# Kernel tuning notes

Hardware: AMD Instinct MI355X
Metric: run time of the kernel (lower is better)

The kernel has to match this reference:

```python
import jax, jax.numpy as jnp
import numpy as np

SPACING = 2
EPS = 1e-8

def setup_inputs() -> dict:
    key = jax.random.key(0)
    x = jax.random.normal(key, (32, 96, 128, 128), dtype=jnp.float32)
    return {"hidden_activations": x}

def reference(hidden_activations):
    s = SPACING
    B, C, H, W = hidden_activations.shape
    ph, pw = H // s, W // s
    R = ph * pw
    # F.unfold(kernel=s, stride=s) -> regions [B,C,R,s*s], kernel positions row-major
    regions = hidden_activations.reshape(B, C, ph, s, pw, s)
    regions = regions.transpose(0, 1, 2, 4, 3, 5).reshape(B, C, R, s * s)
    # append null (no-winner) logit = 0
    aug = jnp.concatenate([regions, jnp.zeros((B, C, R, 1), regions.dtype)], axis=-1)
    # stabilized softmax with +eps in denominator (as in torch code)
    m = jnp.max(aug, axis=-1, keepdims=True)
    e = jnp.exp(aug - m)
    probs = e / (jnp.sum(e, axis=-1, keepdims=True) + EPS)  # [B,C,R,s*s+1]
    # Gumbel-argmax sampling of one winner per region (or null)
    gkey = jax.random.key(1)
    u = jax.random.uniform(gkey, probs.shape, dtype=probs.dtype)
    gumbel = -jnp.log(-jnp.log(u + EPS) + EPS)
    winner = jnp.argmax(jnp.log(probs + EPS) + gumbel, axis=-1)  # [B,C,R]
    # probability value at winner location
    winner_prob = jnp.take_along_axis(probs, winner[..., None], axis=-1)  # [B,C,R,1]
    # scatter winner prob into full-resolution sparse map; winner==s*s (null) -> all zeros
    onehot = (winner[..., None] == jnp.arange(s * s)).astype(probs.dtype)  # [B,C,R,s*s]
    sparse = (onehot * winner_prob).reshape(B, C, ph, pw, s, s)
    sparse = sparse.transpose(0, 1, 2, 4, 3, 5).reshape(B, C, H, W)
    # MATLAB HPc: sum of non-null probs per region
    pooled = jnp.sum(probs[..., :-1], axis=-1).reshape(B, C, ph, pw)
    winner_indices = winner.reshape(B, C, ph, pw)
    return sparse, pooled, winner_indices
```

## Files before the change

kernel.cpp:

```cpp
#include <hip/hip_runtime.h>
#include <stdint.h>

static constexpr uint32_t kBC       = 32u * 96u;
static constexpr uint32_t kR        = 64u * 64u;
static constexpr uint32_t kImg      = 128u * 128u;
static constexpr uint32_t kSparseN  = kBC * kImg;
static constexpr uint32_t kPooledN  = kBC * kR;

#define EPSF 1e-8f

__device__ __forceinline__ uint32_t rotl32(uint32_t v, int r) {
    return (v << r) | (v >> (32 - r));
}

__device__ __forceinline__ void threefry2x32_01(uint32_t x0, uint32_t x1,
                                                uint32_t& o0, uint32_t& o1) {
    const uint32_t ks0 = 0u;
    const uint32_t ks1 = 1u;
    const uint32_t ks2 = 0x1BD11BDAu ^ 0u ^ 1u;
    x0 += ks0; x1 += ks1;
    x0 += x1; x1 = rotl32(x1, 13); x1 ^= x0;
    x0 += x1; x1 = rotl32(x1, 15); x1 ^= x0;
    x0 += x1; x1 = rotl32(x1, 26); x1 ^= x0;
    x0 += x1; x1 = rotl32(x1,  6); x1 ^= x0;
    x0 += ks1; x1 += ks2 + 1u;
    x0 += x1; x1 = rotl32(x1, 17); x1 ^= x0;
    x0 += x1; x1 = rotl32(x1, 29); x1 ^= x0;
    x0 += x1; x1 = rotl32(x1, 16); x1 ^= x0;
    x0 += x1; x1 = rotl32(x1, 24); x1 ^= x0;
    x0 += ks2; x1 += ks0 + 2u;
    x0 += x1; x1 = rotl32(x1, 13); x1 ^= x0;
    x0 += x1; x1 = rotl32(x1, 15); x1 ^= x0;
    x0 += x1; x1 = rotl32(x1, 26); x1 ^= x0;
    x0 += x1; x1 = rotl32(x1,  6); x1 ^= x0;
    x0 += ks0; x1 += ks1 + 3u;
    x0 += x1; x1 = rotl32(x1, 17); x1 ^= x0;
    x0 += x1; x1 = rotl32(x1, 29); x1 ^= x0;
    x0 += x1; x1 = rotl32(x1, 16); x1 ^= x0;
    x0 += x1; x1 = rotl32(x1, 24); x1 ^= x0;
    x0 += ks1; x1 += ks2 + 4u;
    x0 += x1; x1 = rotl32(x1, 13); x1 ^= x0;
    x0 += x1; x1 = rotl32(x1, 15); x1 ^= x0;
    x0 += x1; x1 = rotl32(x1, 26); x1 ^= x0;
    x0 += x1; x1 = rotl32(x1,  6); x1 ^= x0;
    x0 += ks2; x1 += ks0 + 5u;
    o0 = x0; o1 = x1;
}

__device__ __forceinline__ uint32_t jax_bits_partitionable(uint32_t i) {
    uint32_t o0, o1;
    threefry2x32_01(0u, i, o0, o1);
    return o0 ^ o1;
}

__device__ __forceinline__ float gumbel_from_bits(uint32_t bits) {
    uint32_t fb = (bits >> 9) | 0x3F800000u;
    float u = __uint_as_float(fb) - 1.0f;
    float nl = -logf(u + EPSF);
    return -logf(nl + EPSF);
}

__device__ __forceinline__ void do_region_fused(float v0, float v1, float v2, float v3,
                                                uint32_t jbase5,
                                                float& s0, float& s1, float& s2, float& s3,
                                                float& pooledv, float& winv) {
    float g0 = gumbel_from_bits(jax_bits_partitionable(jbase5 + 0u));
    float g1 = gumbel_from_bits(jax_bits_partitionable(jbase5 + 1u));
    float g2 = gumbel_from_bits(jax_bits_partitionable(jbase5 + 2u));
    float g3 = gumbel_from_bits(jax_bits_partitionable(jbase5 + 3u));
    float g4 = gumbel_from_bits(jax_bits_partitionable(jbase5 + 4u));

    float m = fmaxf(fmaxf(fmaxf(fmaxf(v0, v1), v2), v3), 0.0f);
    float e0 = expf(v0 - m);
    float e1 = expf(v1 - m);
    float e2 = expf(v2 - m);
    float e3 = expf(v3 - m);
    float e4 = expf(0.0f - m);
    float den = ((((e0 + e1) + e2) + e3) + e4) + EPSF;
    float p0 = e0 / den;
    float p1 = e1 / den;
    float p2 = e2 / den;
    float p3 = e3 / den;
    float p4 = e4 / den;
    float z0 = logf(p0 + EPSF) + g0;
    float z1 = logf(p1 + EPSF) + g1;
    float z2 = logf(p2 + EPSF) + g2;
    float z3 = logf(p3 + EPSF) + g3;
    float z4 = logf(p4 + EPSF) + g4;
    int w = 0; float best = z0;
    if (z1 > best) { best = z1; w = 1; }
    if (z2 > best) { best = z2; w = 2; }
    if (z3 > best) { best = z3; w = 3; }
    if (z4 > best) { best = z4; w = 4; }
    float wp = (w == 0) ? p0 : (w == 1) ? p1 : (w == 2) ? p2 : (w == 3) ? p3 : p4;
    s0 = (w == 0) ? wp : 0.0f;
    s1 = (w == 1) ? wp : 0.0f;
    s2 = (w == 2) ? wp : 0.0f;
    s3 = (w == 3) ? wp : 0.0f;
    pooledv = ((p0 + p1) + p2) + p3;
    winv = (float)w;
}

__global__ __launch_bounds__(256, 6) void mmp_kernel(const float* __restrict__ x,
                                                     float* __restrict__ sparse,
                                                     float* __restrict__ pooled,
                                                     float* __restrict__ winner) {
    const uint32_t t  = blockIdx.x * 256u + threadIdx.x;
    const uint32_t pj = t & 15u;
    const uint32_t pi = (t >> 4) & 63u;
    const uint32_t bc = t >> 10;

    const float* xp = x + (size_t)bc * kImg + pi * 256u + pj * 8u;
    float4 a0 = *(const float4*)(xp);
    float4 a1 = *(const float4*)(xp + 4);
    float4 b0 = *(const float4*)(xp + 128);
    float4 b1 = *(const float4*)(xp + 132);

    const uint32_t r0    = bc * kR + pi * 64u + pj * 4u;
    const uint32_t jbase = r0 * 5u;
    float* sp = sparse + (size_t)bc * kImg + pi * 256u + pj * 8u;

    float s0, s1, s2, s3;
    float pool0, pool1, pool2, pool3, win0, win1, win2, win3;

    do_region_fused(a0.x, a0.y, b0.x, b0.y, jbase,       s0, s1, s2, s3, pool0, win0);
    *(float2*)(sp)           = make_float2(s0, s1);
    *(float2*)(sp + 128)     = make_float2(s2, s3);
    do_region_fused(a0.z, a0.w, b0.z, b0.w, jbase + 5u,  s0, s1, s2, s3, pool1, win1);
    *(float2*)(sp + 2)       = make_float2(s0, s1);
    *(float2*)(sp + 130)     = make_float2(s2, s3);
    do_region_fused(a1.x, a1.y, b1.x, b1.y, jbase + 10u, s0, s1, s2, s3, pool2, win2);
    *(float2*)(sp + 4)       = make_float2(s0, s1);
    *(float2*)(sp + 132)     = make_float2(s2, s3);
    do_region_fused(a1.z, a1.w, b1.z, b1.w, jbase + 15u, s0, s1, s2, s3, pool3, win3);
    *(float2*)(sp + 6)       = make_float2(s0, s1);
    *(float2*)(sp + 134)     = make_float2(s2, s3);

    *(float4*)(pooled + r0) = make_float4(pool0, pool1, pool2, pool3);
    *(float4*)(winner + r0) = make_float4(win0, win1, win2, win3);
}

extern "C" void kernel_launch(void* const* d_in, const int* in_sizes, int n_in,
                              void* d_out, int out_size, void* d_ws, size_t ws_size,
                              hipStream_t stream) {
    (void)in_sizes; (void)n_in; (void)d_ws; (void)ws_size; (void)out_size;
    const float* x = (const float*)d_in[0];
    float* out = (float*)d_out;
    float* sparse = out;
    float* pooled = out + kSparseN;
    float* winner = out + kSparseN + kPooledN;

    const uint32_t nThreads = kBC * 64u * 16u;
    dim3 grid(nThreads / 256u), block(256u);
    hipLaunchKernelGGL(mmp_kernel, grid, block, 0, stream, x, sparse, pooled, winner);
}
```

Before: 491.7 us.

## Use hardware log2/exp2/rcp fast path with exact fixup pass for ambiguous regions

Replaces precise expf/logf/division in the main kernel with the AMD hardware exp2, log2 and reciprocal intrinsics, and computes the Gumbel-argmax in log2 space. Regions where the top-two margin is small, the input spread is large, or a uniform sample is near zero are pushed onto a workspace list through an atomic counter. A second kernel recomputes those regions with full-precision math to keep the reference winners. This adds a memset, an extra launch and atomic contention in exchange for cheaper transcendental math, and if the list overflows its capacity some regions are left on the approximate path.

```diff
diff --git a/kernel.cpp b/kernel.cpp
--- a/kernel.cpp
+++ b/kernel.cpp
@@ -8,6 +8,9 @@
 static constexpr uint32_t kPooledN  = kBC * kR;
 
 #define EPSF 1e-8f
+#define GAP_THR2 2e-3f
+#define SPREAD_THR 7.0f
+#define TMIN_THR 1e-5f
 
 __device__ __forceinline__ uint32_t rotl32(uint32_t v, int r) {
     return (v << r) | (v >> (32 - r));
@@ -53,45 +56,74 @@
     return o0 ^ o1;
 }
 
-__device__ __forceinline__ float gumbel_from_bits(uint32_t bits) {
+__device__ __forceinline__ float uniform_from_bits(uint32_t bits) {
     uint32_t fb = (bits >> 9) | 0x3F800000u;
-    float u = __uint_as_float(fb) - 1.0f;
-    float nl = -logf(u + EPSF);
-    return -logf(nl + EPSF);
-}
-
-__device__ __forceinline__ void do_region_fused(float v0, float v1, float v2, float v3,
-                                                uint32_t jbase5,
-                                                float& s0, float& s1, float& s2, float& s3,
-                                                float& pooledv, float& winv) {
-    float g0 = gumbel_from_bits(jax_bits_partitionable(jbase5 + 0u));
-    float g1 = gumbel_from_bits(jax_bits_partitionable(jbase5 + 1u));
-    float g2 = gumbel_from_bits(jax_bits_partitionable(jbase5 + 2u));
-    float g3 = gumbel_from_bits(jax_bits_partitionable(jbase5 + 3u));
-    float g4 = gumbel_from_bits(jax_bits_partitionable(jbase5 + 4u));
-
-    float m = fmaxf(fmaxf(fmaxf(fmaxf(v0, v1), v2), v3), 0.0f);
-    float e0 = expf(v0 - m);
-    float e1 = expf(v1 - m);
-    float e2 = expf(v2 - m);
-    float e3 = expf(v3 - m);
-    float e4 = expf(0.0f - m);
+    return __uint_as_float(fb) - 1.0f;
+}
+
+__device__ __forceinline__ float hw_log2(float x) { return __builtin_amdgcn_logf(x); }
+__device__ __forceinline__ float hw_exp2(float x) { return __builtin_amdgcn_exp2f(x); }
+__device__ __forceinline__ float hw_rcp (float x) { return __builtin_amdgcn_rcpf(x); }
+
+__device__ __forceinline__ void do_region_v5(float v0, float v1, float v2, float v3,
+                                             uint32_t rIdx,
+                                             uint32_t* wcount, uint32_t* wlist, uint32_t cap,
+                                             float& s0, float& s1, float& s2, float& s3,
+                                             float& pooledv, float& winv) {
+    const uint32_t jb = rIdx * 5u;
+    float u0 = uniform_from_bits(jax_bits_partitionable(jb + 0u));
+    float u1 = uniform_from_bits(jax_bits_partitionable(jb + 1u));
+    float u2 = uniform_from_bits(jax_bits_partitionable(jb + 2u));
+    float u3 = uniform_from_bits(jax_bits_partitionable(jb + 3u));
+    float u4 = uniform_from_bits(jax_bits_partitionable(jb + 4u));
+
+    const float L2E  = 1.44269504088896340736f;
+    const float NLN2 = -0.69314718055994530942f;
+
+    float m    = fmaxf(fmaxf(fmaxf(fmaxf(v0, v1), v2), v3), 0.0f);
+    float vmin = fminf(fminf(v0, v1), fminf(v2, v3));
+    float c0 = v0 * L2E, c1 = v1 * L2E, c2 = v2 * L2E, c3 = v3 * L2E;
+    float cm = m * L2E;
+
+    float e0 = hw_exp2(c0 - cm);
+    float e1 = hw_exp2(c1 - cm);
+    float e2 = hw_exp2(c2 - cm);
+    float e3 = hw_exp2(c3 - cm);
+    float e4 = hw_exp2(0.0f - cm);
     float den = ((((e0 + e1) + e2) + e3) + e4) + EPSF;
-    float p0 = e0 / den;
-    float p1 = e1 / den;
-    float p2 = e2 / den;
-    float p3 = e3 / den;
-    float p4 = e4 / den;
-    float z0 = logf(p0 + EPSF) + g0;
-    float z1 = logf(p1 + EPSF) + g1;
-    float z2 = logf(p2 + EPSF) + g2;
-    float z3 = logf(p3 + EPSF) + g3;
-    float z4 = logf(p4 + EPSF) + g4;
-    int w = 0; float best = z0;
-    if (z1 > best) { best = z1; w = 1; }
-    if (z2 > best) { best = z2; w = 2; }
-    if (z3 > best) { best = z3; w = 3; }
-    if (z4 > best) { best = z4; w = 4; }
+    float rr  = hw_rcp(den);
+    float p0 = e0 * rr;
+    float p1 = e1 * rr;
+    float p2 = e2 * rr;
+    float p3 = e3 * rr;
+    float p4 = e4 * rr;
+
+    float t0 = fmaf(NLN2, hw_log2(u0 + EPSF), EPSF);
+    float t1 = fmaf(NLN2, hw_log2(u1 + EPSF), EPSF);
+    float t2 = fmaf(NLN2, hw_log2(u2 + EPSF), EPSF);
+    float t3 = fmaf(NLN2, hw_log2(u3 + EPSF), EPSF);
+    float t4 = fmaf(NLN2, hw_log2(u4 + EPSF), EPSF);
+    float z0 = c0 - hw_log2(t0);
+    float z1 = c1 - hw_log2(t1);
+    float z2 = c2 - hw_log2(t2);
+    float z3 = c3 - hw_log2(t3);
+    float z4 = 0.0f - hw_log2(t4);
+    float tmin = fminf(fminf(fminf(t0, t1), fminf(t2, t3)), t4);
+
+    int w = 0; float best = z0; float second = -3.4e38f;
+    if (z1 > best) { second = best; best = z1; w = 1; } else { second = z1; }
+    if (z2 > best) { second = best; best = z2; w = 2; } else if (z2 > second) { second = z2; }
+    if (z3 > best) { second = best; best = z3; w = 3; } else if (z3 > second) { second = z3; }
+    if (z4 > best) { second = best; best = z4; w = 4; } else if (z4 > second) { second = z4; }
+
+    bool flag = (best - second < GAP_THR2) ||
+                (m - fminf(vmin, 0.0f) > SPREAD_THR) ||
+                (tmin < TMIN_THR);
+    if (flag) {
+        uint32_t slot = atomicAdd(wcount, 1u);
+        if (slot < cap) wlist[slot] = rIdx;
+    }
+
     float wp = (w == 0) ? p0 : (w == 1) ? p1 : (w == 2) ? p2 : (w == 3) ? p3 : p4;
     s0 = (w == 0) ? wp : 0.0f;
     s1 = (w == 1) ? wp : 0.0f;
@@ -104,7 +136,10 @@
 __global__ __launch_bounds__(256, 6) void mmp_kernel(const float* __restrict__ x,
                                                      float* __restrict__ sparse,
                                                      float* __restrict__ pooled,
-                                                     float* __restrict__ winner) {
+                                                     float* __restrict__ winner,
+                                                     uint32_t* __restrict__ wcount,
+                                                     uint32_t* __restrict__ wlist,
+                                                     uint32_t cap) {
     const uint32_t t  = blockIdx.x * 256u + threadIdx.x;
     const uint32_t pj = t & 15u;
     const uint32_t pi = (t >> 4) & 63u;
@@ -116,41 +151,104 @@
     float4 b0 = *(const float4*)(xp + 128);
     float4 b1 = *(const float4*)(xp + 132);
 
-    const uint32_t r0    = bc * kR + pi * 64u + pj * 4u;
-    const uint32_t jbase = r0 * 5u;
+    const uint32_t r0 = bc * kR + pi * 64u + pj * 4u;
     float* sp = sparse + (size_t)bc * kImg + pi * 256u + pj * 8u;
 
     float s0, s1, s2, s3;
     float pool0, pool1, pool2, pool3, win0, win1, win2, win3;
 
-    do_region_fused(a0.x, a0.y, b0.x, b0.y, jbase,       s0, s1, s2, s3, pool0, win0);
-    *(float2*)(sp)           = make_float2(s0, s1);
-    *(float2*)(sp + 128)     = make_float2(s2, s3);
-    do_region_fused(a0.z, a0.w, b0.z, b0.w, jbase + 5u,  s0, s1, s2, s3, pool1, win1);
-    *(float2*)(sp + 2)       = make_float2(s0, s1);
-    *(float2*)(sp + 130)     = make_float2(s2, s3);
-    do_region_fused(a1.x, a1.y, b1.x, b1.y, jbase + 10u, s0, s1, s2, s3, pool2, win2);
-    *(float2*)(sp + 4)       = make_float2(s0, s1);
-    *(float2*)(sp + 132)     = make_float2(s2, s3);
-    do_region_fused(a1.z, a1.w, b1.z, b1.w, jbase + 15u, s0, s1, s2, s3, pool3, win3);
-    *(float2*)(sp + 6)       = make_float2(s0, s1);
-    *(float2*)(sp + 134)     = make_float2(s2, s3);
+    do_region_v5(a0.x, a0.y, b0.x, b0.y, r0 + 0u, wcount, wlist, cap, s0, s1, s2, s3, pool0, win0);
+    *(float2*)(sp)       = make_float2(s0, s1);
+    *(float2*)(sp + 128) = make_float2(s2, s3);
+    do_region_v5(a0.z, a0.w, b0.z, b0.w, r0 + 1u, wcount, wlist, cap, s0, s1, s2, s3, pool1, win1);
+    *(float2*)(sp + 2)   = make_float2(s0, s1);
+    *(float2*)(sp + 130) = make_float2(s2, s3);
+    do_region_v5(a1.x, a1.y, b1.x, b1.y, r0 + 2u, wcount, wlist, cap, s0, s1, s2, s3, pool2, win2);
+    *(float2*)(sp + 4)   = make_float2(s0, s1);
+    *(float2*)(sp + 132) = make_float2(s2, s3);
+    do_region_v5(a1.z, a1.w, b1.z, b1.w, r0 + 3u, wcount, wlist, cap, s0, s1, s2, s3, pool3, win3);
+    *(float2*)(sp + 6)   = make_float2(s0, s1);
+    *(float2*)(sp + 134) = make_float2(s2, s3);
 
     *(float4*)(pooled + r0) = make_float4(pool0, pool1, pool2, pool3);
     *(float4*)(winner + r0) = make_float4(win0, win1, win2, win3);
+}
+
+__global__ __launch_bounds__(256) void mmp_fixup(const float* __restrict__ x,
+                                                 float* __restrict__ sparse,
+                                                 float* __restrict__ pooled,
+                                                 float* __restrict__ winner,
+                                                 const uint32_t* __restrict__ wcount,
+                                                 const uint32_t* __restrict__ wlist,
+                                                 uint32_t cap) {
+    uint32_t n = *wcount;
+    if (n > cap) n = cap;
+    for (uint32_t i = blockIdx.x * 256u + threadIdx.x; i < n; i += gridDim.x * 256u) {
+        const uint32_t r    = wlist[i];
+        const uint32_t bc   = r >> 12;
+        const uint32_t rem  = r & 4095u;
+        const uint32_t prow = rem >> 6;
+        const uint32_t pcol = rem & 63u;
+        const size_t base = (size_t)bc * kImg + prow * 256u + pcol * 2u;
+        float v0 = x[base], v1 = x[base + 1u], v2 = x[base + 128u], v3 = x[base + 129u];
+
+        float m  = fmaxf(fmaxf(fmaxf(fmaxf(v0, v1), v2), v3), 0.0f);
+        float e0 = expf(v0 - m);
+        float e1 = expf(v1 - m);
+        float e2 = expf(v2 - m);
+        float e3 = expf(v3 - m);
+        float e4 = expf(0.0f - m);
+        float den = ((((e0 + e1) + e2) + e3) + e4) + EPSF;
+        float p0 = e0 / den, p1 = e1 / den, p2 = e2 / den, p3 = e3 / den, p4 = e4 / den;
+
+        const uint32_t jb = r * 5u;
+        float u0 = uniform_from_bits(jax_bits_partitionable(jb + 0u));
+        float u1 = uniform_from_bits(jax_bits_partitionable(jb + 1u));
+        float u2 = uniform_from_bits(jax_bits_partitionable(jb + 2u));
+        float u3 = uniform_from_bits(jax_bits_partitionable(jb + 3u));
+        float u4 = uniform_from_bits(jax_bits_partitionable(jb + 4u));
+        float y0 = logf(p0 + EPSF) + (-logf(-logf(u0 + EPSF) + EPSF));
+        float y1 = logf(p1 + EPSF) + (-logf(-logf(u1 + EPSF) + EPSF));
+        float y2 = logf(p2 + EPSF) + (-logf(-logf(u2 + EPSF) + EPSF));
+        float y3 = logf(p3 + EPSF) + (-logf(-logf(u3 + EPSF) + EPSF));
+        float y4 = logf(p4 + EPSF) + (-logf(-logf(u4 + EPSF) + EPSF));
+        int w = 0; float best = y0;
+        if (y1 > best) { best = y1; w = 1; }
+        if (y2 > best) { best = y2; w = 2; }
+        if (y3 > best) { best = y3; w = 3; }
+        if (y4 > best) { best = y4; w = 4; }
+        float wp = (w == 0) ? p0 : (w == 1) ? p1 : (w == 2) ? p2 : (w == 3) ? p3 : p4;
+
+        float* sp = sparse + base;
+        sp[0]    = (w == 0) ? wp : 0.0f;
+        sp[1]    = (w == 1) ? wp : 0.0f;
+        sp[128]  = (w == 2) ? wp : 0.0f;
+        sp[129]  = (w == 3) ? wp : 0.0f;
+        pooled[r] = ((p0 + p1) + p2) + p3;
+        winner[r] = (float)w;
+    }
 }
 
 extern "C" void kernel_launch(void* const* d_in, const int* in_sizes, int n_in,
                               void* d_out, int out_size, void* d_ws, size_t ws_size,
                               hipStream_t stream) {
-    (void)in_sizes; (void)n_in; (void)d_ws; (void)ws_size; (void)out_size;
+    (void)in_sizes; (void)n_in; (void)out_size;
     const float* x = (const float*)d_in[0];
     float* out = (float*)d_out;
     float* sparse = out;
     float* pooled = out + kSparseN;
     float* winner = out + kSparseN + kPooledN;
 
+    uint32_t* wcount = (uint32_t*)d_ws;
+    uint32_t* wlist  = (uint32_t*)d_ws + 4;
+    uint32_t cap = (ws_size > 16) ? (uint32_t)((ws_size - 16) / 4) : 0u;
+
+    hipMemsetAsync(d_ws, 0, 4, stream);
+
     const uint32_t nThreads = kBC * 64u * 16u;
     dim3 grid(nThreads / 256u), block(256u);
-    hipLaunchKernelGGL(mmp_kernel, grid, block, 0, stream, x, sparse, pooled, winner);
-}
+    hipLaunchKernelGGL(mmp_kernel, grid, block, 0, stream,
+                       x, sparse, pooled, winner, wcount, wlist, cap);
+    hipLaunchKernelGGL(mmp_fixup, dim3(128), dim3(256), 0, stream,
+                       x, sparse, pooled, winner, wcount, wlist, cap);
+}
```

New measurement: 493.9 us. About the same (+0.4%).
